# Kernel tuning notes

Hardware: AMD Instinct MI355X
Metric: run time of the kernel (lower is better)

## Reference

```python
import jax, jax.numpy as jnp
import numpy as np
import math

B, S, HID, H = 2, 2048, 1024, 16
D = HID // H  # head_dim = 64

def _get_slopes(n):
    # power-of-2 branch (n=16)
    start = 2 ** (-2 ** (-(math.log2(n) - 3)))
    return np.array([start * 2 ** (-i) for i in range(n)], dtype=np.float32)

def setup_inputs() -> dict:
    key = jax.random.key(0)
    ks = jax.random.split(key, 9)
    sc = 1.0 / math.sqrt(HID)
    return {
        "x":  jax.random.normal(ks[0], (B, S, HID), dtype=jnp.float32),
        "Wq": jax.random.normal(ks[1], (HID, HID), dtype=jnp.float32) * sc,
        "bq": jnp.zeros((HID,), dtype=jnp.float32),
        "Wk": jax.random.normal(ks[2], (HID, HID), dtype=jnp.float32) * sc,
        "bk": jnp.zeros((HID,), dtype=jnp.float32),
        "Wv": jax.random.normal(ks[3], (HID, HID), dtype=jnp.float32) * sc,
        "bv": jnp.zeros((HID,), dtype=jnp.float32),
        "Wo": jax.random.normal(ks[4], (HID, HID), dtype=jnp.float32) * sc,
        "bo": jnp.zeros((HID,), dtype=jnp.float32),
        "slopes": jnp.asarray(_get_slopes(H)),
    }

def reference(x, Wq, bq, Wk, bk, Wv, bv, Wo, bo, slopes):
    b, s, hid = x.shape
    h = slopes.shape[0]
    d = hid // h
    # projections (torch Linear: y = x @ W.T + b), split heads -> [b,h,s,d]
    q = (x @ Wq.T + bq).reshape(b, s, h, d).transpose(0, 2, 1, 3)
    k = (x @ Wk.T + bk).reshape(b, s, h, d).transpose(0, 2, 1, 3)
    v = (x @ Wv.T + bv).reshape(b, s, h, d).transpose(0, 2, 1, 3)
    scores = jnp.einsum('bhqd,bhkd->bhqk', q, k) / jnp.sqrt(jnp.float32(d))
    # ALiBi bias: slope_h * (j - i), shape [h,s,s]
    pos = jnp.arange(s)
    dist = (pos[None, :] - pos[:, None]).astype(x.dtype)  # [s,s]
    scores = scores + slopes[None, :, None, None] * dist[None, None]
    attn = jax.nn.softmax(scores, axis=-1)
    ctx = jnp.einsum('bhqk,bhkd->bhqd', attn, v)
    ctx = ctx.transpose(0, 2, 1, 3).reshape(b, s, hid)
    return ctx @ Wo.T + bo
```

## Files before the change

### kernel.cpp

```cpp
#include <hip/hip_runtime.h>
#include <stdint.h>

typedef __attribute__((ext_vector_type(8))) short bf16x8;
typedef __attribute__((ext_vector_type(4))) short bf16x4;
typedef __attribute__((ext_vector_type(4))) float f32x4;
typedef unsigned short u16t;

#define DEVINL static __device__ __forceinline__

DEVINL u16t f2bf(float f) {
  union { float f; unsigned u; } v; v.f = f;
  return (u16t)((v.u + 0x7FFFu + ((v.u >> 16) & 1u)) >> 16);
}

DEVINL float exp2_fast(float x) {
  float r; asm("v_exp_f32 %0, %1" : "=v"(r) : "v"(x)); return r;
}
DEVINL unsigned cvt_pk_bf16(float a, float b) {
  unsigned r; asm("v_cvt_pk_bf16_f32 %0, %1, %2" : "=v"(r) : "v"(a), "v"(b)); return r;
}
DEVINL float max3f(float a, float b, float c) {
  float r; asm("v_max3_f32 %0, %1, %2, %3" : "=v"(r) : "v"(a), "v"(b), "v"(c)); return r;
}

DEVINL void gload16(const void* g, void* l) {
  __builtin_amdgcn_global_load_lds((const __attribute__((address_space(1))) void*)g,
                                   (__attribute__((address_space(3))) void*)l, 16, 0, 0);
}

__global__ __launch_bounds__(256)
void cvt5_kernel(const float* __restrict__ x, const float* __restrict__ wq,
                 const float* __restrict__ wk, const float* __restrict__ wv,
                 const float* __restrict__ wo, u16t* __restrict__ x_bf,
                 u16t* __restrict__ wqkv, u16t* __restrict__ wo_bf) {
  const int bid = blockIdx.x;
  const float* src; u16t* dst; int off;
  if (bid < 2048) { src = x; dst = x_bf; off = bid * 2048; }
  else {
    const int j = bid - 2048, sel = j >> 9;
    off = (j & 511) * 2048;
    if (sel == 0)      { src = wq; dst = wqkv; }
    else if (sel == 1) { src = wk; dst = wqkv + 1048576; }
    else if (sel == 2) { src = wv; dst = wqkv + 2097152; }
    else               { src = wo; dst = wo_bf; }
  }
  const int i = off + threadIdx.x * 8;
  float4 a = *(const float4*)(src + i);
  float4 b = *(const float4*)(src + i + 4);
  union { bf16x8 v; u16t u[8]; } o;
  o.u[0] = f2bf(a.x); o.u[1] = f2bf(a.y); o.u[2] = f2bf(a.z); o.u[3] = f2bf(a.w);
  o.u[4] = f2bf(b.x); o.u[5] = f2bf(b.y); o.u[6] = f2bf(b.z); o.u[7] = f2bf(b.w);
  *(bf16x8*)(dst + i) = o.v;
}

template <int MODE>
__global__ __launch_bounds__(256, 2)
void gemm_kernel(const u16t* __restrict__ A, const u16t* __restrict__ Bw,
                 const float* __restrict__ bias0, const float* __restrict__ bias1,
                 const float* __restrict__ bias2, void* __restrict__ outp) {
  __shared__ __attribute__((aligned(16))) u16t As[128 * 64];
  __shared__ __attribute__((aligned(16))) u16t Bs[128 * 64];
  const int tid = threadIdx.x;
  const int w = tid >> 6, l = tid & 63;
  const int wm = w >> 1, wn = w & 1;
  const int bm = blockIdx.x, bn = blockIdx.y;
  const int g = l >> 4, r16 = l & 15;
  const int srow = l >> 3, sslot = l & 7;

  f32x4 acc[4][4];
#pragma unroll
  for (int m = 0; m < 4; ++m)
#pragma unroll
    for (int n = 0; n < 4; ++n) acc[m][n] = f32x4{0.f, 0.f, 0.f, 0.f};

  const size_t arow0 = (size_t)bm * 128;
  const size_t brow0 = (size_t)bn * 128;

  for (int kt = 0; kt < 16; ++kt) {
    __syncthreads();
#pragma unroll
    for (int i = 0; i < 4; ++i) {
      const int row = (i * 4 + w) * 8 + srow;
      const int colA = kt * 64 + ((sslot ^ (row & 7)) * 8);
      gload16(A + (arow0 + row) * 1024 + colA, (char*)As + (i * 4 + w) * 1024);
      gload16(Bw + (brow0 + row) * 1024 + colA, (char*)Bs + (i * 4 + w) * 1024);
    }
    asm volatile("s_waitcnt vmcnt(0)" ::: "memory");
    __syncthreads();
#pragma unroll
    for (int kk = 0; kk < 2; ++kk) {
      bf16x8 af[4], bfr[4];
#pragma unroll
      for (int m = 0; m < 4; ++m) {
        const int rr = wm * 64 + m * 16 + r16;
        af[m] = *(const bf16x8*)((const char*)As + rr * 128 + (((kk * 4 + g) ^ (rr & 7)) * 16));
      }
#pragma unroll
      for (int n = 0; n < 4; ++n) {
        const int rr = wn * 64 + n * 16 + r16;
        bfr[n] = *(const bf16x8*)((const char*)Bs + rr * 128 + (((kk * 4 + g) ^ (rr & 7)) * 16));
      }
#pragma unroll
      for (int m = 0; m < 4; ++m)
#pragma unroll
        for (int n = 0; n < 4; ++n)
          acc[m][n] = __builtin_amdgcn_mfma_f32_16x16x32_bf16(af[m], bfr[n], acc[m][n], 0, 0, 0);
    }
  }

  if (MODE == 0) {
    const int mat = bn >> 3;
    if (mat == 2) {
      u16t* vt = (u16t*)outp + 8388608u;
#pragma unroll
      for (int n = 0; n < 4; ++n) {
        const int col = ((bn & 7) * 128) + wn * 64 + n * 16 + r16;
        const int hh = col >> 6, dd = col & 63;
        const float bv = bias2[col];
#pragma unroll
        for (int m = 0; m < 4; ++m) {
          const int row0 = bm * 128 + wm * 64 + m * 16 + g * 4;
          const int b_ = row0 >> 11, s_ = row0 & 2047;
          union { bf16x4 v; u16t u[4]; } o4;
#pragma unroll
          for (int i = 0; i < 4; ++i) o4.u[i] = f2bf(acc[m][n][i] + bv);
          *(bf16x4*)(vt + ((size_t)(b_ * 16 + hh) * 64 + dd) * 2048 + s_) = o4.v;
        }
      }
    } else {
      const float* bias = (mat == 0) ? bias0 : bias1;
      const float scale = (mat == 0) ? 0.18033688f : 1.0f;
      u16t* o = (u16t*)outp + (size_t)mat * 4194304u;
#pragma unroll
      for (int n = 0; n < 4; ++n) {
        const int col = ((bn & 7) * 128) + wn * 64 + n * 16 + r16;
        const float bv = bias[col];
#pragma unroll
        for (int m = 0; m < 4; ++m) {
          const int row = bm * 128 + wm * 64 + m * 16 + g * 4;
#pragma unroll
          for (int i = 0; i < 4; ++i)
            o[(size_t)(row + i) * 1024 + col] = f2bf((acc[m][n][i] + bv) * scale);
        }
      }
    }
  } else {
    float* o = (float*)outp;
#pragma unroll
    for (int n = 0; n < 4; ++n) {
      const int col = bn * 128 + wn * 64 + n * 16 + r16;
      const float bv = bias0[col];
#pragma unroll
      for (int m = 0; m < 4; ++m) {
        const int row = bm * 128 + wm * 64 + m * 16 + g * 4;
#pragma unroll
        for (int i = 0; i < 4; ++i)
          o[(size_t)(row + i) * 1024 + col] = acc[m][n][i] + bv;
      }
    }
  }
}

__global__ __launch_bounds__(256, 2)
void attn_kernel(const u16t* __restrict__ Qb, const u16t* __restrict__ Kb,
                 const u16t* __restrict__ Vtb, const float* __restrict__ slopes,
                 u16t* __restrict__ Ctx) {
  __shared__ __attribute__((aligned(16))) u16t Kl[3][2048];
  __shared__ __attribute__((aligned(16))) u16t Vl[3][2048];
  const int tid = threadIdx.x;
  const int w = tid >> 6, l = tid & 63;
  const int g = l >> 4, r = l & 15;
  const int qt = blockIdx.x, bh = blockIdx.y;
  const int b = bh >> 4, h = bh & 15;
  const float slope2 = slopes[h] * 1.44269504f;
  const int qpos = qt * 64 + w * 16 + r;
  const size_t base = (size_t)b * 2097152 + (size_t)h * 64;

  const u16t* qrow = Qb + base + (size_t)qpos * 1024;
  const bf16x8 qf0 = *(const bf16x8*)(qrow + g * 8);
  const bf16x8 qf1 = *(const bf16x8*)(qrow + 32 + g * 8);
  asm volatile("s_waitcnt vmcnt(0)" ::: "memory");

  const int sig = 8 * (r >> 2) + (r & 3);
  const int toffs[2] = {0, 4};
  int koff[2][2], voff[4];
#pragma unroll
  for (int t = 0; t < 2; ++t) {
    const int row = toffs[t] + sig;
    const int mk = (row & 3) ^ ((row >> 1) & 4);
#pragma unroll
    for (int hh = 0; hh < 2; ++hh) koff[t][hh] = row * 128 + (((hh * 4 + g) ^ mk) * 16);
  }
#pragma unroll
  for (int db = 0; db < 4; ++db) {
    const int row = 16 * db + r;
    const int vm = (row & 3) ^ ((row >> 2) & 3);
    voff[db] = row * 64 + ((g ^ vm) * 16);
  }

  const int krow_s = w * 8 + (l >> 3);
  const int ku_s = (((l & 7) ^ ((krow_s & 3) ^ ((krow_s >> 1) & 4)))) * 8;
  const int vrow_s = w * 16 + (l >> 2);
  const int vu_s = (((l & 3) ^ ((vrow_s & 3) ^ ((vrow_s >> 2) & 3)))) * 8;

  f32x4 cv[2];
#pragma unroll
  for (int t = 0; t < 2; ++t)
#pragma unroll
    for (int i = 0; i < 4; ++i) cv[t][i] = slope2 * (float)(toffs[t] + 8 * g + i);

  const float d32 = slope2 * 32.f;
  float mj = -3.0e38f;
  f32x4 oc[4], sacc;
#pragma unroll
  for (int d = 0; d < 4; ++d) oc[d] = f32x4{0.f, 0.f, 0.f, 0.f};
  sacc = f32x4{0.f, 0.f, 0.f, 0.f};
  union { bf16x8 v; u16t u[8]; } ones;
#pragma unroll
  for (int i = 0; i < 8; ++i) ones.u[i] = 0x3F80;

  const u16t* Krow = Kb + base;
  const u16t* Vrow = Vtb + (size_t)(b * 16 + h) * 131072;

#define STAGE(kt_, b_)                                                            \
  {                                                                               \
    gload16(Krow + (size_t)((kt_) * 32 + krow_s) * 1024 + ku_s,                   \
            (char*)Kl + (b_) * 4096 + w * 1024);                                  \
    gload16(Vrow + (size_t)vrow_s * 2048 + (kt_) * 32 + vu_s,                     \
            (char*)Vl + (b_) * 4096 + w * 1024);                                  \
  }

  STAGE(63, 0)
  STAGE(62, 1)

  for (int it = 0; it < 64; ++it) {
    const int kt = 63 - it;
    const int buf = it % 3;
    if (it == 63) { asm volatile("s_waitcnt vmcnt(0)" ::: "memory"); }
    else          { asm volatile("s_waitcnt vmcnt(2)" ::: "memory"); }
    __builtin_amdgcn_s_barrier();
    asm volatile("" ::: "memory");
    const int nkt = (kt >= 2) ? kt - 2 : 0;
    STAGE(nkt, (it + 2) % 3)
    if (it) mj += d32;

    const char* KB = (const char*)Kl + buf * 4096;
    const char* VB = (const char*)Vl + buf * 4096;

    f32x4 st[2];
#pragma unroll
    for (int t = 0; t < 2; ++t) {
      st[t] = __builtin_amdgcn_mfma_f32_16x16x32_bf16(
          *(const bf16x8*)(KB + koff[t][0]), qf0, cv[t], 0, 0, 0);
      st[t] = __builtin_amdgcn_mfma_f32_16x16x32_bf16(
          *(const bf16x8*)(KB + koff[t][1]), qf1, st[t], 0, 0, 0);
    }

    const float m1 = max3f(st[0][0], st[0][1], st[0][2]);
    const float m2 = max3f(st[0][3], st[1][0], st[1][1]);
    const float m3 = max3f(st[1][2], st[1][3], m1);
    const float tm = fmaxf(m2, m3);
    if (__any(tm > mj)) {
      float tr = fmaxf(tm, __shfl_xor(tm, 16));
      tr = fmaxf(tr, __shfl_xor(tr, 32));
      const float mn = fmaxf(mj, tr);
      const float corr = exp2_fast(mj - mn);
#pragma unroll
      for (int d = 0; d < 4; ++d) {
        oc[d][0] *= corr; oc[d][1] *= corr; oc[d][2] *= corr; oc[d][3] *= corr;
      }
      sacc[0] *= corr; sacc[1] *= corr; sacc[2] *= corr; sacc[3] *= corr;
      mj = mn;
    }

    float pe[8];
#pragma unroll
    for (int t = 0; t < 2; ++t)
#pragma unroll
      for (int i = 0; i < 4; ++i) pe[t * 4 + i] = exp2_fast(st[t][i] - mj);
    union { bf16x8 v; unsigned q[4]; } pb;
#pragma unroll
    for (int j = 0; j < 4; ++j) pb.q[j] = cvt_pk_bf16(pe[j * 2], pe[j * 2 + 1]);

#pragma unroll
    for (int db = 0; db < 4; ++db)
      oc[db] = __builtin_amdgcn_mfma_f32_16x16x32_bf16(
          *(const bf16x8*)(VB + voff[db]), pb.v, oc[db], 0, 0, 0);
    sacc = __builtin_amdgcn_mfma_f32_16x16x32_bf16(ones.v, pb.v, sacc, 0, 0, 0);
  }
#undef STAGE

  const float inv = 1.0f / sacc[0];
  u16t* orow = Ctx + base + (size_t)qpos * 1024;
#pragma unroll
  for (int d = 0; d < 4; ++d) {
    union { bf16x4 v; u16t u[4]; } o4;
#pragma unroll
    for (int i = 0; i < 4; ++i) o4.u[i] = f2bf(oc[d][i] * inv);
    *(bf16x4*)(orow + d * 16 + g * 4) = o4.v;
  }
}

extern "C" void kernel_launch(void* const* d_in, const int* in_sizes, int n_in,
                              void* d_out, int out_size, void* d_ws, size_t ws_size,
                              hipStream_t stream) {
  const float* x = (const float*)d_in[0];
  const float* Wq = (const float*)d_in[1];
  const float* bq = (const float*)d_in[2];
  const float* Wk = (const float*)d_in[3];
  const float* bk = (const float*)d_in[4];
  const float* Wv = (const float*)d_in[5];
  const float* bv = (const float*)d_in[6];
  const float* Wo = (const float*)d_in[7];
  const float* bo = (const float*)d_in[8];
  const float* slopes = (const float*)d_in[9];
  if (ws_size < (size_t)(48u << 20)) return;
  char* ws = (char*)d_ws;
  u16t* x_bf = (u16t*)(ws);
  u16t* wqkv = (u16t*)(ws + (8u << 20));
  u16t* wo_bf = (u16t*)(ws + (14u << 20));
  u16t* q_bf = (u16t*)(ws + (16u << 20));
  u16t* ctx_bf = (u16t*)(ws + (40u << 20));

  cvt5_kernel<<<4096, 256, 0, stream>>>(x, Wq, Wk, Wv, Wo, x_bf, wqkv, wo_bf);
  gemm_kernel<0><<<dim3(32, 24), 256, 0, stream>>>(x_bf, wqkv, bq, bk, bv, (void*)q_bf);
  attn_kernel<<<dim3(32, 32), 256, 0, stream>>>(q_bf, q_bf + 4194304, q_bf + 8388608,
                                                slopes, ctx_bf);
  gemm_kernel<1><<<dim3(32, 8), 256, 0, stream>>>(ctx_bf, wo_bf, bo, bo, bo, d_out);
}
```

Baseline: 127.2 us.

## Split attention KV range across two blocks and merge with combine kernel

```diff
diff --git a/kernel.cpp b/kernel.cpp
--- a/kernel.cpp
+++ b/kernel.cpp
@@ -11,6 +11,9 @@
 DEVINL u16t f2bf(float f) {
   union { float f; unsigned u; } v; v.f = f;
   return (u16t)((v.u + 0x7FFFu + ((v.u >> 16) & 1u)) >> 16);
+}
+DEVINL float bf2f(u16t u) {
+  union { unsigned u; float f; } v; v.u = ((unsigned)u) << 16; return v.f;
 }
 
 DEVINL float exp2_fast(float x) {
@@ -164,13 +167,14 @@
 __global__ __launch_bounds__(256, 2)
 void attn_kernel(const u16t* __restrict__ Qb, const u16t* __restrict__ Kb,
                  const u16t* __restrict__ Vtb, const float* __restrict__ slopes,
-                 u16t* __restrict__ Ctx) {
+                 u16t* __restrict__ O0, u16t* __restrict__ O1,
+                 float2* __restrict__ ML) {
   __shared__ __attribute__((aligned(16))) u16t Kl[3][2048];
-  __shared__ __attribute__((aligned(16))) u16t Vl[3][2048];
+  __shared__ __attribute__((aligned(16))) u16t Vl[2][2048];
   const int tid = threadIdx.x;
   const int w = tid >> 6, l = tid & 63;
   const int g = l >> 4, r = l & 15;
-  const int qt = blockIdx.x, bh = blockIdx.y;
+  const int qt = blockIdx.x, bh = blockIdx.y, sp = blockIdx.z;
   const int b = bh >> 4, h = bh & 15;
   const float slope2 = slopes[h] * 1.44269504f;
   const int qpos = qt * 64 + w * 16 + r;
@@ -192,16 +196,14 @@
     for (int hh = 0; hh < 2; ++hh) koff[t][hh] = row * 128 + (((hh * 4 + g) ^ mk) * 16);
   }
 #pragma unroll
-  for (int db = 0; db < 4; ++db) {
-    const int row = 16 * db + r;
-    const int vm = (row & 3) ^ ((row >> 2) & 3);
-    voff[db] = row * 64 + ((g ^ vm) * 16);
-  }
-
-  const int krow_s = w * 8 + (l >> 3);
-  const int ku_s = (((l & 7) ^ ((krow_s & 3) ^ ((krow_s >> 1) & 4)))) * 8;
-  const int vrow_s = w * 16 + (l >> 2);
-  const int vu_s = (((l & 3) ^ ((vrow_s & 3) ^ ((vrow_s >> 2) & 3)))) * 8;
+  for (int db = 0; db < 4; ++db)
+    voff[db] = (8 * db + (r >> 1)) * 128 + ((((((r & 1) << 2) | g)) ^ ((r >> 1) & 3)) * 16);
+
+  const int kline_s = w * 8 + (l >> 3);
+  const int ku_s = ((l & 7) ^ ((kline_s & 3) ^ ((kline_s >> 1) & 4))) * 8;
+  const int vu_s = (l & 7) ^ (kline_s & 3);
+  const int vd_s = 2 * kline_s + (vu_s >> 2);
+  const int vcol_s = (vu_s & 3) * 8;
 
   f32x4 cv[2];
 #pragma unroll
@@ -221,31 +223,32 @@
 
   const u16t* Krow = Kb + base;
   const u16t* Vrow = Vtb + (size_t)(b * 16 + h) * 131072;
-
-#define STAGE(kt_, b_)                                                            \
-  {                                                                               \
-    gload16(Krow + (size_t)((kt_) * 32 + krow_s) * 1024 + ku_s,                   \
-            (char*)Kl + (b_) * 4096 + w * 1024);                                  \
-    gload16(Vrow + (size_t)vrow_s * 2048 + (kt_) * 32 + vu_s,                     \
-            (char*)Vl + (b_) * 4096 + w * 1024);                                  \
-  }
-
-  STAGE(63, 0)
-  STAGE(62, 1)
-
-  for (int it = 0; it < 64; ++it) {
-    const int kt = 63 - it;
-    const int buf = it % 3;
-    if (it == 63) { asm volatile("s_waitcnt vmcnt(0)" ::: "memory"); }
-    else          { asm volatile("s_waitcnt vmcnt(2)" ::: "memory"); }
+  const int kt0 = sp * 32 + 31;
+
+#define STAGE_K(kt_, b_)                                                          \
+  gload16(Krow + (size_t)((kt_) * 32 + kline_s) * 1024 + ku_s,                    \
+          (char*)Kl + (b_) * 4096 + w * 1024);
+#define STAGE_V(kt_, b_)                                                          \
+  gload16(Vrow + (size_t)vd_s * 2048 + (kt_) * 32 + vcol_s,                       \
+          (char*)Vl + (b_) * 4096 + w * 1024);
+
+  STAGE_K(kt0, 0)
+  STAGE_V(kt0, 0)
+  STAGE_K(kt0 - 1, 1)
+
+  for (int it = 0; it < 32; ++it) {
+    const int kt = kt0 - it;
+    const int kbuf = it % 3, vbuf = it & 1;
+    if (it == 31) { asm volatile("s_waitcnt vmcnt(0)" ::: "memory"); }
+    else          { asm volatile("s_waitcnt vmcnt(1)" ::: "memory"); }
     __builtin_amdgcn_s_barrier();
     asm volatile("" ::: "memory");
-    const int nkt = (kt >= 2) ? kt - 2 : 0;
-    STAGE(nkt, (it + 2) % 3)
+    if (it + 1 < 32) STAGE_V(kt - 1, vbuf ^ 1)
+    if (it + 2 < 32) STAGE_K(kt - 2, (it + 2) % 3)
     if (it) mj += d32;
 
-    const char* KB = (const char*)Kl + buf * 4096;
-    const char* VB = (const char*)Vl + buf * 4096;
+    const char* KB = (const char*)Kl + kbuf * 4096;
+    const char* VB = (const char*)Vl + vbuf * 4096;
 
     f32x4 st[2];
 #pragma unroll
@@ -288,17 +291,41 @@
           *(const bf16x8*)(VB + voff[db]), pb.v, oc[db], 0, 0, 0);
     sacc = __builtin_amdgcn_mfma_f32_16x16x32_bf16(ones.v, pb.v, sacc, 0, 0, 0);
   }
-#undef STAGE
-
-  const float inv = 1.0f / sacc[0];
-  u16t* orow = Ctx + base + (size_t)qpos * 1024;
+#undef STAGE_K
+#undef STAGE_V
+
+  u16t* op = (sp ? O1 : O0) + base + (size_t)qpos * 1024;
 #pragma unroll
   for (int d = 0; d < 4; ++d) {
     union { bf16x4 v; u16t u[4]; } o4;
 #pragma unroll
-    for (int i = 0; i < 4; ++i) o4.u[i] = f2bf(oc[d][i] * inv);
-    *(bf16x4*)(orow + d * 16 + g * 4) = o4.v;
-  }
+    for (int i = 0; i < 4; ++i) o4.u[i] = f2bf(oc[d][i]);
+    *(bf16x4*)(op + d * 16 + g * 4) = o4.v;
+  }
+  if (l < 16) {
+    const float m_global = mj + (sp ? slope2 * 1024.f : 0.f);
+    ML[((size_t)(sp * 2 + b) * 16 + h) * 2048 + qpos] = float2{m_global, sacc[0]};
+  }
+}
+
+__global__ __launch_bounds__(256)
+void combine_kernel(u16t* __restrict__ O0 ,
+                    const u16t* __restrict__ O1, const float2* __restrict__ ML) {
+  const int idx = blockIdx.x * 256 + threadIdx.x;
+  const int colg = idx & 127, tok = idx >> 7;
+  const int b = tok >> 11, s = tok & 2047, h = colg >> 3;
+  const float2 ml0 = ML[((size_t)(0 + b) * 16 + h) * 2048 + s];
+  const float2 ml1 = ML[((size_t)(2 + b) * 16 + h) * 2048 + s];
+  const float M = fmaxf(ml0.x, ml1.x);
+  const float e0 = exp2_fast(ml0.x - M), e1 = exp2_fast(ml1.x - M);
+  const float invL = 1.f / (ml0.y * e0 + ml1.y * e1);
+  const float w0 = e0 * invL, w1 = e1 * invL;
+  union { bf16x8 v; u16t u[8]; } a, c, o;
+  a.v = *(const bf16x8*)(O0 + (size_t)idx * 8);
+  c.v = *(const bf16x8*)(O1 + (size_t)idx * 8);
+#pragma unroll
+  for (int i = 0; i < 8; ++i) o.u[i] = f2bf(bf2f(a.u[i]) * w0 + bf2f(c.u[i]) * w1);
+  *(bf16x8*)(O0 + (size_t)idx * 8) = o.v;
 }
 
 extern "C" void kernel_launch(void* const* d_in, const int* in_sizes, int n_in,
@@ -321,10 +348,13 @@
   u16t* wo_bf = (u16t*)(ws + (14u << 20));
   u16t* q_bf = (u16t*)(ws + (16u << 20));
   u16t* ctx_bf = (u16t*)(ws + (40u << 20));
+  u16t* part1 = (u16t*)(ws);
+  float2* ml = (float2*)(ws + (8u << 20));
 
   cvt5_kernel<<<4096, 256, 0, stream>>>(x, Wq, Wk, Wv, Wo, x_bf, wqkv, wo_bf);
   gemm_kernel<0><<<dim3(32, 24), 256, 0, stream>>>(x_bf, wqkv, bq, bk, bv, (void*)q_bf);
-  attn_kernel<<<dim3(32, 32), 256, 0, stream>>>(q_bf, q_bf + 4194304, q_bf + 8388608,
-                                                slopes, ctx_bf);
+  attn_kernel<<<dim3(32, 32, 2), 256, 0, stream>>>(q_bf, q_bf + 4194304, q_bf + 8388608,
+                                                   slopes, ctx_bf, part1, ml);
+  combine_kernel<<<2048, 256, 0, stream>>>(ctx_bf, part1, ml);
   gemm_kernel<1><<<dim3(32, 8), 256, 0, stream>>>(ctx_bf, wo_bf, bo, bo, bo, d_out);
 }
```

Result: slower. 129.9 us (+2.1%).
